# Performance work log

Hardware: AMD Instinct MI355X
Metric: run time of the kernel (lower is better)

The kernel has to match this reference:

```python
import jax, jax.numpy as jnp
import numpy as np

N_NODES = 50000
N_FEAT = 128
DIM = 10
N_EDGES = 1600000
N_GRAPHS = 1000


def setup_inputs() -> dict:
    key = jax.random.key(0)
    ks = jax.random.split(key, 8)
    x = jax.random.normal(ks[0], (N_NODES, N_FEAT), dtype=jnp.float32)
    W1_l = jax.random.normal(ks[1], (DIM, N_FEAT), dtype=jnp.float32) * 0.1
    W1_r = jax.random.normal(ks[2], (DIM, N_FEAT), dtype=jnp.float32) * 0.1
    W2_l = jax.random.normal(ks[3], (DIM, DIM), dtype=jnp.float32) * 0.3
    W2_r = jax.random.normal(ks[4], (DIM, DIM), dtype=jnp.float32) * 0.3
    Wfc = jax.random.normal(ks[5], (1, DIM), dtype=jnp.float32) * 0.3
    edge_index = jax.random.randint(ks[6], (2, N_EDGES), 0, N_NODES, dtype=jnp.int64)
    batch = jnp.sort(jax.random.randint(ks[7], (N_NODES,), 0, N_GRAPHS, dtype=jnp.int64))
    return {"x": x, "W1_l": W1_l, "W1_r": W1_r, "W2_l": W2_l, "W2_r": W2_r,
            "Wfc": Wfc, "edge_index": edge_index, "batch": batch}


def _sage_conv(h, src, dst, deg_inv, Wl, Wr):
    # mean aggregation over incoming neighbors, then two bias-free linears
    agg = jax.ops.segment_sum(h[src], dst, num_segments=N_NODES)  # [N, F]
    agg = agg * deg_inv[:, None]
    return agg @ Wl.T + h @ Wr.T


def reference(x, W1_l, W1_r, W2_l, W2_r, Wfc, edge_index, batch):
    src, dst = edge_index[0], edge_index[1]
    # in-degree per destination node (mean denominator, clamped at 1 like PyG)
    deg = jax.ops.segment_sum(jnp.ones((src.shape[0],), x.dtype), dst, num_segments=N_NODES)
    deg_inv = 1.0 / jnp.maximum(deg, 1.0)

    h = jax.nn.relu(_sage_conv(x, src, dst, deg_inv, W1_l, W1_r))
    h = _sage_conv(h, src, dst, deg_inv, W2_l, W2_r)

    # global mean pool over graphs
    counts = jax.ops.segment_sum(jnp.ones((N_NODES,), x.dtype), batch, num_segments=N_GRAPHS)
    pooled = jax.ops.segment_sum(h, batch, num_segments=N_GRAPHS)
    pooled = pooled / jnp.maximum(counts, 1.0)[:, None]

    return jax.nn.sigmoid(pooled @ Wfc.T)  # [N_GRAPHS, 1]
```

## Files before the change

kernel.cpp:

```cpp
#include <hip/hip_runtime.h>
#include <hip/hip_bf16.h>
#include <math.h>

#define N_NODES  50000
#define N_FEAT   128
#define DIM      10
#define N_EDGES  1600000
#define N_GRAPHS 1000
#define PSTRIDE  16
#define CAP      80
#define BSH      8
#define NBUCK    196
#define BCAP     9216
#define ACHUNK   4096
#define ABLOCKS  ((N_EDGES + ACHUNK - 1) / ACHUNK)
#define PBLOCKS  ((N_NODES + 255) / 256)
#define SPLIT    8
#define GSLOTS   128

__device__ __forceinline__ float bf2f(unsigned short u) {
    union { unsigned int i; float f; } v;
    v.i = ((unsigned int)u) << 16;
    return v.f;
}

__device__ __forceinline__ float wload(const void* w, int fm, int i) {
    return fm ? ((const float*)w)[i] : bf2f(((const unsigned short*)w)[i]);
}

__device__ __forceinline__ int iload(const void* p, int im, long long pos) {
    return im ? (int)((const long long*)p)[pos] : ((const int*)p)[pos];
}

__global__ void detect_setup_kernel(
    const unsigned short* __restrict__ w1l, const unsigned int* __restrict__ ei32,
    const void* __restrict__ W2l, const void* __restrict__ W2r,
    const void* __restrict__ Wfc,
    int* __restrict__ fmode, int* __restrict__ imode,
    float* __restrict__ vl, float* __restrict__ vr,
    int* __restrict__ bcur, float* __restrict__ gsum, float* __restrict__ gcnt) {
    __shared__ int bigcnt, oddnz;
    if (threadIdx.x == 0) { bigcnt = 0; oddnz = 0; }
    __syncthreads();
    for (int i = threadIdx.x; i < DIM * N_FEAT; i += 256) {
        int expo = (w1l[i] >> 7) & 0xFF;
        if (expo >= 0x90) atomicAdd(&bigcnt, 1);
    }
    for (int i = threadIdx.x; i < 2048; i += 256) {
        if (ei32[2 * i + 1] != 0) atomicAdd(&oddnz, 1);
    }
    for (int i = threadIdx.x; i < NBUCK; i += 256) bcur[i] = 0;
    for (int i = threadIdx.x; i < N_GRAPHS; i += 256) { gsum[i] = 0.f; gcnt[i] = 0.f; }
    __syncthreads();
    int fm = (bigcnt >= 4) ? 1 : 0;
    if (threadIdx.x == 0) { *fmode = fm; *imode = (oddnz == 0) ? 1 : 0; }
    int j = threadIdx.x;
    if (j < DIM) {
        float al = 0.f, ar = 0.f;
        for (int i = 0; i < DIM; i++) {
            float w = wload(Wfc, fm, i);
            al += w * wload(W2l, fm, i * DIM + j);
            ar += w * wload(W2r, fm, i * DIM + j);
        }
        vl[j] = al;
        vr[j] = ar;
    } else if (j < 16) {
        vl[j] = 0.f;
        vr[j] = 0.f;
    }
}

#define ACCUM8(f0)                                                  \
    _Pragma("unroll")                                               \
    for (int d = 0; d < DIM; d++) {                                 \
        _Pragma("unroll")                                           \
        for (int k = 0; k < 8; k++) {                               \
            accl[d] += xf[k] * wl[d * N_FEAT + (f0) + k];           \
            accr[d] += xf[k] * wr[d * N_FEAT + (f0) + k];           \
        }                                                           \
    }

__global__ __launch_bounds__(256) void fusedA_kernel(
    const void* __restrict__ ei, const void* __restrict__ x,
    const void* __restrict__ W1l, const void* __restrict__ W1r,
    const int* __restrict__ fmode, const int* __restrict__ imode,
    int* __restrict__ bcur, unsigned int* __restrict__ bedges,
    float* __restrict__ p, float* __restrict__ q) {
    __shared__ union U {
        struct { unsigned int stage[ACHUNK]; int hcnt[NBUCK]; int hbase[NBUCK]; } a;
        struct { float wl[DIM * N_FEAT]; float wr[DIM * N_FEAT]; } b;
    } sh;

    if (blockIdx.x < ABLOCKS) {
        int im = *imode;
        for (int b = threadIdx.x; b < NBUCK; b += 256) sh.a.hcnt[b] = 0;
        __syncthreads();
        long long e0 = (long long)blockIdx.x * ACHUNK;
        int nE = (int)min((long long)ACHUNK, (long long)N_EDGES - e0);
        for (int i = threadIdx.x; i < nE; i += 256) {
            int s = iload(ei, im, e0 + i);
            int d = iload(ei, im, (long long)N_EDGES + e0 + i);
            sh.a.stage[i] = (unsigned)s | ((unsigned)(d & 255) << 16) | ((unsigned)(d >> BSH) << 24);
            atomicAdd(&sh.a.hcnt[d >> BSH], 1);
        }
        __syncthreads();
        for (int b = threadIdx.x; b < NBUCK; b += 256) {
            int c = sh.a.hcnt[b];
            sh.a.hbase[b] = c ? atomicAdd(&bcur[b], c) : 0;
            sh.a.hcnt[b] = 0;
        }
        __syncthreads();
        for (int i = threadIdx.x; i < nE; i += 256) {
            unsigned rec = sh.a.stage[i];
            int b = rec >> 24;
            int pos = sh.a.hbase[b] + atomicAdd(&sh.a.hcnt[b], 1);
            if (pos < BCAP) bedges[(size_t)b * BCAP + pos] = rec;
        }
    } else {
        int fm = *fmode;
        float* wl = sh.b.wl;
        float* wr = sh.b.wr;
        for (int i = threadIdx.x; i < DIM * N_FEAT; i += 256) {
            wl[i] = wload(W1l, fm, i);
            wr[i] = wload(W1r, fm, i);
        }
        __syncthreads();
        int n = (blockIdx.x - ABLOCKS) * 256 + threadIdx.x;
        if (n >= N_NODES) return;

        float accl[DIM], accr[DIM];
#pragma unroll
        for (int d = 0; d < DIM; d++) { accl[d] = 0.f; accr[d] = 0.f; }

        if (fm) {
            const float4* xr = reinterpret_cast<const float4*>((const float*)x + (size_t)n * N_FEAT);
            for (int fb = 0; fb < N_FEAT / 8; fb++) {
                float4 v0 = xr[2 * fb];
                float4 v1 = xr[2 * fb + 1];
                float xf[8] = {v0.x, v0.y, v0.z, v0.w, v1.x, v1.y, v1.z, v1.w};
                ACCUM8(fb * 8)
            }
        } else {
            const uint4* xr = reinterpret_cast<const uint4*>((const unsigned short*)x + (size_t)n * N_FEAT);
            for (int fb = 0; fb < N_FEAT / 8; fb++) {
                uint4 v = xr[fb];
                float xf[8];
                xf[0] = bf2f((unsigned short)(v.x & 0xffff)); xf[1] = bf2f((unsigned short)(v.x >> 16));
                xf[2] = bf2f((unsigned short)(v.y & 0xffff)); xf[3] = bf2f((unsigned short)(v.y >> 16));
                xf[4] = bf2f((unsigned short)(v.z & 0xffff)); xf[5] = bf2f((unsigned short)(v.z >> 16));
                xf[6] = bf2f((unsigned short)(v.w & 0xffff)); xf[7] = bf2f((unsigned short)(v.w >> 16));
                ACCUM8(fb * 8)
            }
        }
        float* pr = p + (size_t)n * PSTRIDE;
        float* qr = q + (size_t)n * PSTRIDE;
#pragma unroll
        for (int d = 0; d < DIM; d++) { pr[d] = accl[d]; qr[d] = accr[d]; }
#pragma unroll
        for (int d = DIM; d < PSTRIDE; d++) { pr[d] = 0.f; qr[d] = 0.f; }
    }
}

__global__ __launch_bounds__(1024) void binB_kernel(
    const int* __restrict__ bcur, const unsigned int* __restrict__ bedges,
    int* __restrict__ cnt, unsigned short* __restrict__ col) {
    __shared__ unsigned short lcol[256 * CAP];
    __shared__ int lcnt[256];
    int b = blockIdx.x;
    if (threadIdx.x < 256) lcnt[threadIdx.x] = 0;
    __syncthreads();
    int m = min(bcur[b], BCAP);
    const unsigned int* seg = bedges + (size_t)b * BCAP;
    for (int i = threadIdx.x; i < m; i += 1024) {
        unsigned rec = seg[i];
        int nidx = (rec >> 16) & 255;
        int pos = atomicAdd(&lcnt[nidx], 1);
        if (pos < CAP) lcol[nidx * CAP + pos] = (unsigned short)(rec & 0xffffu);
    }
    __syncthreads();
    int node0 = b << BSH;
    int nvalid = min(256, N_NODES - node0);
    if ((int)threadIdx.x < nvalid) cnt[node0 + threadIdx.x] = lcnt[threadIdx.x];
    int total = nvalid * CAP / 8;
    uint4* dst4 = (uint4*)(col + (size_t)node0 * CAP);
    const uint4* src4 = (const uint4*)lcol;
    for (int i = threadIdx.x; i < total; i += 1024) dst4[i] = src4[i];
}

__global__ __launch_bounds__(256) void pull1_kernel(
    const int* __restrict__ cnt, const unsigned short* __restrict__ col,
    const float* __restrict__ p, const float* __restrict__ q,
    const float* __restrict__ vl, const float* __restrict__ vr,
    float* __restrict__ t, float* __restrict__ u, float* __restrict__ dinv) {
    int g = blockIdx.x * 16 + (threadIdx.x >> 4);
    int sub = threadIdx.x & 15;
    if (g >= N_NODES) return;
    int deg = cnt[g];
    int dcl = min(deg, CAP);
    const unsigned short* cl = col + (size_t)g * CAP;
    float acc = 0.f;
    for (int k0 = 0; k0 < dcl; k0 += 8) {
        uint4 cv = *reinterpret_cast<const uint4*>(cl + k0);
        int cs[8];
        cs[0] = cv.x & 0xffff; cs[1] = cv.x >> 16;
        cs[2] = cv.y & 0xffff; cs[3] = cv.y >> 16;
        cs[4] = cv.z & 0xffff; cs[5] = cv.z >> 16;
        cs[6] = cv.w & 0xffff; cs[7] = cv.w >> 16;
#pragma unroll
        for (int j = 0; j < 8; j++) {
            float v = p[(size_t)cs[j] * PSTRIDE + sub];
            acc += (k0 + j < dcl) ? v : 0.f;
        }
    }
    float di = 1.0f / fmaxf((float)deg, 1.0f);
    float h = fmaxf(acc * di + q[(size_t)g * PSTRIDE + sub], 0.f);
    float tv = h * vl[sub];
    float uv = h * vr[sub];
#pragma unroll
    for (int off = 8; off > 0; off >>= 1) {
        tv += __shfl_xor(tv, off, 16);
        uv += __shfl_xor(uv, off, 16);
    }
    if (sub == 0) {
        t[g] = tv;
        u[g] = uv;
        dinv[g] = di;
    }
}

__global__ __launch_bounds__(256) void pull2B_kernel(
    const int* __restrict__ bcur, const unsigned int* __restrict__ bedges,
    const float* __restrict__ t, const float* __restrict__ u,
    const float* __restrict__ dinv, const void* __restrict__ batch,
    const int* __restrict__ imode,
    float* __restrict__ gsum, float* __restrict__ gcnt) {
    __shared__ float ldinv[256];
    __shared__ int   lb[256];
    __shared__ float lgs[GSLOTS];
    __shared__ float lgc[GSLOTS];
    int b = blockIdx.x / SPLIT;
    int s = blockIdx.x % SPLIT;
    int tid = threadIdx.x;
    int node0 = b << BSH;
    int nvalid = min(256, N_NODES - node0);
    int im = *imode;
    if (tid < nvalid) {
        ldinv[tid] = dinv[node0 + tid];
        lb[tid] = iload(batch, im, node0 + tid);
    }
    if (tid < GSLOTS) { lgs[tid] = 0.f; lgc[tid] = 0.f; }
    __syncthreads();
    int g0 = lb[0];
    int rng = lb[nvalid - 1] - g0 + 1;
    bool useLDS = (rng <= GSLOTS);
    int m = min(bcur[b], BCAP);
    int c0 = (m * s) / SPLIT, c1 = (m * (s + 1)) / SPLIT;
    const unsigned int* seg = bedges + (size_t)b * BCAP;
    for (int i = c0 + tid; i < c1; i += 256) {
        unsigned rec = seg[i];
        int src  = rec & 0xffffu;
        int nidx = (rec >> 16) & 255;
        float val = t[src] * ldinv[nidx];
        int gg = lb[nidx];
        if (useLDS) atomicAdd(&lgs[gg - g0], val);
        else        atomicAdd(gsum + gg, val);
    }
    if (s == 0 && tid < nvalid) {
        int gg = lb[tid];
        float uval = u[node0 + tid];
        if (useLDS) {
            atomicAdd(&lgs[gg - g0], uval);
            atomicAdd(&lgc[gg - g0], 1.0f);
        } else {
            atomicAdd(gsum + gg, uval);
            atomicAdd(gcnt + gg, 1.0f);
        }
    }
    __syncthreads();
    if (useLDS) {
        for (int i = tid; i < rng; i += 256) {
            float v = lgs[i];
            if (v != 0.f) atomicAdd(gsum + g0 + i, v);
            if (s == 0) {
                float c = lgc[i];
                if (c != 0.f) atomicAdd(gcnt + g0 + i, c);
            }
        }
    }
}

__global__ __launch_bounds__(256) void final_kernel(
    const float* __restrict__ gsum, const float* __restrict__ gcnt,
    const int* __restrict__ fmode, void* __restrict__ out) {
    int g = blockIdx.x * 256 + threadIdx.x;
    if (g >= N_GRAPHS) return;
    float pooled = gsum[g] / fmaxf(gcnt[g], 1.0f);
    float sg = 1.0f / (1.0f + expf(-pooled));
    if (*fmode) {
        ((float*)out)[g] = sg;
    } else {
        ((__hip_bfloat16*)out)[g] = __float2bfloat16(sg);
    }
}

extern "C" void kernel_launch(void* const* d_in, const int* in_sizes, int n_in,
                              void* d_out, int out_size, void* d_ws, size_t ws_size,
                              hipStream_t stream) {
    const void* x    = d_in[0];
    const void* W1l  = d_in[1];
    const void* W1r  = d_in[2];
    const void* W2l  = d_in[3];
    const void* W2r  = d_in[4];
    const void* Wfc  = d_in[5];
    const void* ei   = d_in[6];
    const void* batc = d_in[7];

    char* ws = (char*)d_ws;
    int*   fmode = (int*)ws;
    int*   imode = fmode + 1;
    float* vl   = (float*)(ws + 64);
    float* vr   = vl + 16;
    int*   bcur = (int*)(vr + 16);
    float* gsum = (float*)(bcur + NBUCK);
    float* gcnt = gsum + N_GRAPHS;
    unsigned int* bedges = (unsigned int*)(ws + ((((size_t)(gcnt + N_GRAPHS) - (size_t)ws) + 255) & ~(size_t)255));
    int*   cnt  = (int*)(bedges + (size_t)NBUCK * BCAP);
    unsigned short* col = (unsigned short*)(cnt + N_NODES);
    float* p    = (float*)(col + (size_t)N_NODES * CAP);
    float* q    = p + (size_t)N_NODES * PSTRIDE;
    float* t    = q + (size_t)N_NODES * PSTRIDE;
    float* u    = t + N_NODES;
    float* dinv = u + N_NODES;

    detect_setup_kernel<<<1, 256, 0, stream>>>(
        (const unsigned short*)W1l, (const unsigned int*)ei, W2l, W2r, Wfc,
        fmode, imode, vl, vr, bcur, gsum, gcnt);
    fusedA_kernel<<<ABLOCKS + PBLOCKS, 256, 0, stream>>>(
        ei, x, W1l, W1r, fmode, imode, bcur, bedges, p, q);
    binB_kernel<<<NBUCK, 1024, 0, stream>>>(bcur, bedges, cnt, col);
    pull1_kernel<<<(N_NODES * 16 + 255) / 256, 256, 0, stream>>>(cnt, col, p, q, vl, vr, t, u, dinv);
    pull2B_kernel<<<NBUCK * SPLIT, 256, 0, stream>>>(bcur, bedges, t, u, dinv, batc, imode, gsum, gcnt);
    final_kernel<<<(N_GRAPHS + 255) / 256, 256, 0, stream>>>(gsum, gcnt, fmode, d_out);
}
```

Before: 165.4 us.

## Vectorize pull1 gathers with float4, pad columns with sentinel, fuse final into pull2B

pull1 now uses 4 threads per node, each gathering a float4 of the neighbour's 16-float row, instead of 16 threads each reading one scalar. Unused column slots are filled with a sentinel node whose p row is zero, so the per-edge bounds mask goes away. The final sigmoid kernel is folded into pull2B: the last block to finish, found through an atomic ticket counter, computes the output, which saves one launch. ACHUNK is doubled, halving the number of edge-binning blocks, and binB now also pays for a full LDS sentinel fill.

Measured after the change: 255.6 us. +54.6%, slower.

```diff
diff --git a/kernel.cpp b/kernel.cpp
--- a/kernel.cpp
+++ b/kernel.cpp
@@ -12,11 +12,12 @@
 #define BSH      8
 #define NBUCK    196
 #define BCAP     9216
-#define ACHUNK   4096
+#define ACHUNK   8192
 #define ABLOCKS  ((N_EDGES + ACHUNK - 1) / ACHUNK)
 #define PBLOCKS  ((N_NODES + 255) / 256)
 #define SPLIT    8
 #define GSLOTS   128
+#define SENT     50000
 
 __device__ __forceinline__ float bf2f(unsigned short u) {
     union { unsigned int i; float f; } v;
@@ -38,7 +39,8 @@
     const void* __restrict__ Wfc,
     int* __restrict__ fmode, int* __restrict__ imode,
     float* __restrict__ vl, float* __restrict__ vr,
-    int* __restrict__ bcur, float* __restrict__ gsum, float* __restrict__ gcnt) {
+    int* __restrict__ bcur, float* __restrict__ gsum, float* __restrict__ gcnt,
+    int* __restrict__ dcount, float* __restrict__ p) {
     __shared__ int bigcnt, oddnz;
     if (threadIdx.x == 0) { bigcnt = 0; oddnz = 0; }
     __syncthreads();
@@ -51,6 +53,8 @@
     }
     for (int i = threadIdx.x; i < NBUCK; i += 256) bcur[i] = 0;
     for (int i = threadIdx.x; i < N_GRAPHS; i += 256) { gsum[i] = 0.f; gcnt[i] = 0.f; }
+    if (threadIdx.x < PSTRIDE) p[(size_t)SENT * PSTRIDE + threadIdx.x] = 0.f;
+    if (threadIdx.x == 32) *dcount = 0;
     __syncthreads();
     int fm = (bigcnt >= 4) ? 1 : 0;
     if (threadIdx.x == 0) { *fmode = fm; *imode = (oddnz == 0) ? 1 : 0; }
@@ -166,9 +170,13 @@
     int* __restrict__ cnt, unsigned short* __restrict__ col) {
     __shared__ unsigned short lcol[256 * CAP];
     __shared__ int lcnt[256];
+    const unsigned int s2 = (unsigned)SENT | ((unsigned)SENT << 16);
+    uint4 sv = make_uint4(s2, s2, s2, s2);
+    uint4* l4 = reinterpret_cast<uint4*>(lcol);
+    for (int i = threadIdx.x; i < 256 * CAP * 2 / 16; i += 1024) l4[i] = sv;
+    if (threadIdx.x < 256) lcnt[threadIdx.x] = 0;
+    __syncthreads();
     int b = blockIdx.x;
-    if (threadIdx.x < 256) lcnt[threadIdx.x] = 0;
-    __syncthreads();
     int m = min(bcur[b], BCAP);
     const unsigned int* seg = bedges + (size_t)b * BCAP;
     for (int i = threadIdx.x; i < m; i += 1024) {
@@ -192,36 +200,39 @@
     const float* __restrict__ p, const float* __restrict__ q,
     const float* __restrict__ vl, const float* __restrict__ vr,
     float* __restrict__ t, float* __restrict__ u, float* __restrict__ dinv) {
-    int g = blockIdx.x * 16 + (threadIdx.x >> 4);
-    int sub = threadIdx.x & 15;
+    int g = blockIdx.x * 64 + (threadIdx.x >> 2);
+    int sub4 = (threadIdx.x & 3) * 4;
     if (g >= N_NODES) return;
     int deg = cnt[g];
     int dcl = min(deg, CAP);
     const unsigned short* cl = col + (size_t)g * CAP;
-    float acc = 0.f;
+    float ax = 0.f, ay = 0.f, az = 0.f, aw = 0.f;
     for (int k0 = 0; k0 < dcl; k0 += 8) {
         uint4 cv = *reinterpret_cast<const uint4*>(cl + k0);
-        int cs[8];
-        cs[0] = cv.x & 0xffff; cs[1] = cv.x >> 16;
-        cs[2] = cv.y & 0xffff; cs[3] = cv.y >> 16;
-        cs[4] = cv.z & 0xffff; cs[5] = cv.z >> 16;
-        cs[6] = cv.w & 0xffff; cs[7] = cv.w >> 16;
+        unsigned c[8];
+        c[0] = cv.x & 0xffff; c[1] = cv.x >> 16;
+        c[2] = cv.y & 0xffff; c[3] = cv.y >> 16;
+        c[4] = cv.z & 0xffff; c[5] = cv.z >> 16;
+        c[6] = cv.w & 0xffff; c[7] = cv.w >> 16;
 #pragma unroll
         for (int j = 0; j < 8; j++) {
-            float v = p[(size_t)cs[j] * PSTRIDE + sub];
-            acc += (k0 + j < dcl) ? v : 0.f;
+            const float4 v = *reinterpret_cast<const float4*>(p + (size_t)c[j] * PSTRIDE + sub4);
+            ax += v.x; ay += v.y; az += v.z; aw += v.w;
         }
     }
     float di = 1.0f / fmaxf((float)deg, 1.0f);
-    float h = fmaxf(acc * di + q[(size_t)g * PSTRIDE + sub], 0.f);
-    float tv = h * vl[sub];
-    float uv = h * vr[sub];
-#pragma unroll
-    for (int off = 8; off > 0; off >>= 1) {
-        tv += __shfl_xor(tv, off, 16);
-        uv += __shfl_xor(uv, off, 16);
-    }
-    if (sub == 0) {
+    float4 qv  = *reinterpret_cast<const float4*>(q + (size_t)g * PSTRIDE + sub4);
+    float4 vlv = *reinterpret_cast<const float4*>(vl + sub4);
+    float4 vrv = *reinterpret_cast<const float4*>(vr + sub4);
+    float hx = fmaxf(ax * di + qv.x, 0.f);
+    float hy = fmaxf(ay * di + qv.y, 0.f);
+    float hz = fmaxf(az * di + qv.z, 0.f);
+    float hw = fmaxf(aw * di + qv.w, 0.f);
+    float tv = hx * vlv.x + hy * vlv.y + hz * vlv.z + hw * vlv.w;
+    float uv = hx * vrv.x + hy * vrv.y + hz * vrv.z + hw * vrv.w;
+    tv += __shfl_xor(tv, 1, 4); tv += __shfl_xor(tv, 2, 4);
+    uv += __shfl_xor(uv, 1, 4); uv += __shfl_xor(uv, 2, 4);
+    if (sub4 == 0) {
         t[g] = tv;
         u[g] = uv;
         dinv[g] = di;
@@ -233,11 +244,14 @@
     const float* __restrict__ t, const float* __restrict__ u,
     const float* __restrict__ dinv, const void* __restrict__ batch,
     const int* __restrict__ imode,
-    float* __restrict__ gsum, float* __restrict__ gcnt) {
+    float* __restrict__ gsum, float* __restrict__ gcnt,
+    int* __restrict__ dcount, const int* __restrict__ fmode,
+    void* __restrict__ out) {
     __shared__ float ldinv[256];
     __shared__ int   lb[256];
     __shared__ float lgs[GSLOTS];
     __shared__ float lgc[GSLOTS];
+    __shared__ int ticket;
     int b = blockIdx.x / SPLIT;
     int s = blockIdx.x % SPLIT;
     int tid = threadIdx.x;
@@ -287,19 +301,19 @@
             }
         }
     }
-}
-
-__global__ __launch_bounds__(256) void final_kernel(
-    const float* __restrict__ gsum, const float* __restrict__ gcnt,
-    const int* __restrict__ fmode, void* __restrict__ out) {
-    int g = blockIdx.x * 256 + threadIdx.x;
-    if (g >= N_GRAPHS) return;
-    float pooled = gsum[g] / fmaxf(gcnt[g], 1.0f);
-    float sg = 1.0f / (1.0f + expf(-pooled));
-    if (*fmode) {
-        ((float*)out)[g] = sg;
-    } else {
-        ((__hip_bfloat16*)out)[g] = __float2bfloat16(sg);
+    __threadfence();
+    if (tid == 0) ticket = atomicAdd(dcount, 1);
+    __syncthreads();
+    if (ticket == NBUCK * SPLIT - 1) {
+        int fm = *fmode;
+        for (int g = tid; g < N_GRAPHS; g += 256) {
+            float sgs = atomicAdd(gsum + g, 0.0f);
+            float cgs = atomicAdd(gcnt + g, 0.0f);
+            float pooled = sgs / fmaxf(cgs, 1.0f);
+            float sg = 1.0f / (1.0f + expf(-pooled));
+            if (fm) ((float*)out)[g] = sg;
+            else    ((__hip_bfloat16*)out)[g] = __float2bfloat16(sg);
+        }
     }
 }
 
@@ -323,22 +337,23 @@
     int*   bcur = (int*)(vr + 16);
     float* gsum = (float*)(bcur + NBUCK);
     float* gcnt = gsum + N_GRAPHS;
-    unsigned int* bedges = (unsigned int*)(ws + ((((size_t)(gcnt + N_GRAPHS) - (size_t)ws) + 255) & ~(size_t)255));
+    int*   dcount = (int*)(gcnt + N_GRAPHS);
+    unsigned int* bedges = (unsigned int*)(ws + ((((size_t)(dcount + 1) - (size_t)ws) + 255) & ~(size_t)255));
     int*   cnt  = (int*)(bedges + (size_t)NBUCK * BCAP);
     unsigned short* col = (unsigned short*)(cnt + N_NODES);
     float* p    = (float*)(col + (size_t)N_NODES * CAP);
-    float* q    = p + (size_t)N_NODES * PSTRIDE;
+    float* q    = p + (size_t)(N_NODES + 1) * PSTRIDE;
     float* t    = q + (size_t)N_NODES * PSTRIDE;
     float* u    = t + N_NODES;
     float* dinv = u + N_NODES;
 
     detect_setup_kernel<<<1, 256, 0, stream>>>(
         (const unsigned short*)W1l, (const unsigned int*)ei, W2l, W2r, Wfc,
-        fmode, imode, vl, vr, bcur, gsum, gcnt);
+        fmode, imode, vl, vr, bcur, gsum, gcnt, dcount, p);
     fusedA_kernel<<<ABLOCKS + PBLOCKS, 256, 0, stream>>>(
         ei, x, W1l, W1r, fmode, imode, bcur, bedges, p, q);
     binB_kernel<<<NBUCK, 1024, 0, stream>>>(bcur, bedges, cnt, col);
-    pull1_kernel<<<(N_NODES * 16 + 255) / 256, 256, 0, stream>>>(cnt, col, p, q, vl, vr, t, u, dinv);
-    pull2B_kernel<<<NBUCK * SPLIT, 256, 0, stream>>>(bcur, bedges, t, u, dinv, batc, imode, gsum, gcnt);
-    final_kernel<<<(N_GRAPHS + 255) / 256, 256, 0, stream>>>(gsum, gcnt, fmode, d_out);
-}
+    pull1_kernel<<<(N_NODES * 4 + 255) / 256, 256, 0, stream>>>(cnt, col, p, q, vl, vr, t, u, dinv);
+    pull2B_kernel<<<NBUCK * SPLIT, 256, 0, stream>>>(bcur, bedges, t, u, dinv, batc, imode,
+                                                     gsum, gcnt, dcount, fmode, d_out);
+}
```
